# Optimization experiments

Hardware: AMD Instinct MI355X
Metric: run time of the kernel (lower is better)

The kernel has to match this reference:

```python
import jax, jax.numpy as jnp
import numpy as np

N, E = 100000, 1200000
IN, HC = 3, 64
FC1, FC2, FC3, OUT = 64, 32, 16, 3
BN_EPS = 1e-5


def _lin(key, fan_in, fan_out):
    # kaiming-uniform-ish init, zero bias (as in parameter_init)
    bound = np.sqrt(6.0 / fan_in)
    w = jax.random.uniform(key, (fan_in, fan_out), minval=-bound, maxval=bound, dtype=jnp.float32)
    return w, jnp.zeros((fan_out,), jnp.float32)


def setup_inputs() -> dict:
    key = jax.random.key(0)
    ks = jax.random.split(key, 16)
    x = jax.random.normal(ks[0], (N, IN), dtype=jnp.float32)
    edge_index = jax.random.randint(ks[1], (2, E), 0, N, dtype=jnp.int64)
    d = {"x": x, "edge_index": edge_index}
    # EdgeConv MLPs: Linear(2*c_in, hc) -> ReLU -> Linear(hc, hc)
    d["w1a"], d["b1a"] = _lin(ks[2], 2 * IN, HC)
    d["w1b"], d["b1b"] = _lin(ks[3], HC, HC)
    d["w2a"], d["b2a"] = _lin(ks[4], 2 * HC, HC)
    d["w2b"], d["b2b"] = _lin(ks[5], HC, HC)
    d["w3a"], d["b3a"] = _lin(ks[6], 2 * HC, HC)
    d["w3b"], d["b3b"] = _lin(ks[7], HC, HC)
    # BatchNorm (eval mode) params per layer: gamma, beta, running_mean, running_var
    for i in (1, 2, 3):
        d[f"bn{i}_g"] = jnp.ones((HC,), jnp.float32)
        d[f"bn{i}_b"] = jnp.zeros((HC,), jnp.float32)
        d[f"bn{i}_m"] = jnp.zeros((HC,), jnp.float32)
        d[f"bn{i}_v"] = jnp.ones((HC,), jnp.float32)
    # dense head
    d["lw1"], d["lb1"] = _lin(ks[8], HC, FC1)
    d["lw2"], d["lb2"] = _lin(ks[9], FC1, FC2)
    d["lw3"], d["lb3"] = _lin(ks[10], FC2, FC3)
    d["lw4"], d["lb4"] = _lin(ks[11], FC3, OUT)
    return d


def _edge_conv(x, src, dst, wa, ba, wb, bb):
    # PyG EdgeConv: message = mlp(cat[x_i, x_j - x_i]), max-aggregated at target i
    x_i = x[dst]                              # [E, C]
    x_j = x[src]                              # [E, C]
    h = jnp.concatenate([x_i, x_j - x_i], axis=-1)   # [E, 2C]
    h = jax.nn.relu(h @ wa + ba) @ wb + bb           # [E, HC]
    agg = jax.ops.segment_max(h, dst, num_segments=x.shape[0])
    return jnp.where(jnp.isfinite(agg), agg, 0.0)    # isolated nodes -> 0


def _bn(x, g, b, m, v):
    return (x - m) * jax.lax.rsqrt(v + BN_EPS) * g + b


def reference(x, edge_index,
              w1a, b1a, w1b, b1b, w2a, b2a, w2b, b2b, w3a, b3a, w3b, b3b,
              bn1_g, bn1_b, bn1_m, bn1_v, bn2_g, bn2_b, bn2_m, bn2_v,
              bn3_g, bn3_b, bn3_m, bn3_v,
              lw1, lb1, lw2, lb2, lw3, lb3, lw4, lb4):
    src, dst = edge_index[0], edge_index[1]
    h = _edge_conv(x, src, dst, w1a, b1a, w1b, b1b)
    h = jax.nn.relu(_bn(h, bn1_g, bn1_b, bn1_m, bn1_v))
    h = _edge_conv(h, src, dst, w2a, b2a, w2b, b2b)
    h = jax.nn.relu(_bn(h, bn2_g, bn2_b, bn2_m, bn2_v))
    h = _edge_conv(h, src, dst, w3a, b3a, w3b, b3b)
    h = jax.nn.relu(_bn(h, bn3_g, bn3_b, bn3_m, bn3_v))
    h = jax.nn.relu(h @ lw1 + lb1)
    h = jax.nn.relu(h @ lw2 + lb2)
    h = jax.nn.relu(h @ lw3 + lb3)
    return h @ lw4 + lb4
```

## Files before the change

kernel.cpp:

```cpp
#include <hip/hip_runtime.h>

#define CAP 64
#define BN_EPS 1e-5f

typedef _Float16 f16;
typedef _Float16 half8 __attribute__((ext_vector_type(8)));
typedef float f32x4 __attribute__((ext_vector_type(4)));

__global__ __launch_bounds__(256) void build_buckets(
    const int* __restrict__ ei, int E,
    int* __restrict__ deg, int* __restrict__ bucket)
{
    int e = blockIdx.x * blockDim.x + threadIdx.x;
    if (e >= E) return;
    int src = ei[e];
    int dst = ei[E + e];
    int slot = atomicAdd(&deg[dst], 1);
    if (slot < CAP) bucket[dst * CAP + slot] = src;
}

__global__ __launch_bounds__(256) void uv_kernel(
    const float* __restrict__ feat, int ldf, int K, int N,
    const float* __restrict__ wa, const float* __restrict__ ba,
    f16* __restrict__ U, f16* __restrict__ V)
{
    __shared__ float Wlds[2][64][64];
    __shared__ float blds[64];
    int tid = threadIdx.x;
    for (int idx = tid; idx < 2 * K * 64; idx += blockDim.x) {
        int half = idx / (K * 64);
        int rem = idx - half * (K * 64);
        int k = rem >> 6, o = rem & 63;
        float wB = wa[(K + k) * 64 + o];
        Wlds[half][k][o] = (half == 0) ? (wa[k * 64 + o] - wB) : wB;
    }
    if (tid < 64) blds[tid] = ba[tid];
    __syncthreads();

    int t = blockIdx.x * blockDim.x + tid;
    if (t >= 2 * N) return;
    int node = t >> 1, half = t & 1;

    float acc[64];
    #pragma unroll
    for (int o = 0; o < 64; ++o) acc[o] = (half == 0) ? blds[o] : 0.f;

    const float* f = feat + (long)node * ldf;
    for (int k = 0; k < K; ++k) {
        float c = f[k];
        #pragma unroll
        for (int o = 0; o < 64; ++o) acc[o] = fmaf(c, Wlds[half][k][o], acc[o]);
    }
    f16* dstp = (half == 0 ? U : V) + (long)node * 64;
    #pragma unroll
    for (int o = 0; o < 64; o += 8) {
        half8 h;
        #pragma unroll
        for (int j = 0; j < 8; ++j) h[j] = (f16)acc[o + j];
        *(half8*)(dstp + o) = h;
    }
}

__global__ __launch_bounds__(256) void node_kernel(
    const f16* __restrict__ U, const f16* __restrict__ V,
    const int* __restrict__ deg, const int* __restrict__ bucket,
    const float* __restrict__ wb, const float* __restrict__ bb,
    const float* __restrict__ bng, const float* __restrict__ bnb,
    const float* __restrict__ bnm, const float* __restrict__ bnv,
    int N, float* __restrict__ Fout)
{
    const int lane = threadIdx.x & 63;
    const int r16 = lane >> 4, c16 = lane & 15;
    const int wid = (blockIdx.x * blockDim.x + threadIdx.x) >> 6;
    const int nwaves = (gridDim.x * blockDim.x) >> 6;

    half8 bfrag[8];
    #pragma unroll
    for (int ct = 0; ct < 4; ++ct)
        #pragma unroll
        for (int s = 0; s < 2; ++s) {
            half8 h;
            #pragma unroll
            for (int j = 0; j < 8; ++j) {
                int k = 32 * s + 8 * r16 + j;
                h[j] = (f16)wb[k * 64 + 16 * ct + c16];
            }
            bfrag[ct * 2 + s] = h;
        }

    const float bbv = bb[lane];
    const float g = bng[lane], be = bnb[lane];
    const float rs = rsqrtf(bnv[lane] + BN_EPS), mm = bnm[lane];

    int chunk = (N + nwaves - 1) / nwaves;
    int n0 = wid * chunk;
    int n1 = n0 + chunk; if (n1 > N) n1 = N;

    for (int node = n0; node < n1; ++node) {
        int d = deg[node]; if (d > CAP) d = CAP;

        const half8* urow = (const half8*)(U + (long)node * 64);
        half8 u0 = urow[r16];
        half8 u1 = urow[4 + r16];

        float m0 = -INFINITY, m1 = -INFINITY, m2 = -INFINITY, m3 = -INFINITY;
        int ntile = (d + 15) >> 4;
        for (int t = 0; t < ntile; ++t) {
            int slot = t * 16 + c16;
            int src = (slot < d) ? bucket[node * CAP + slot] : 0;
            const half8* vrow = (const half8*)(V + (long)src * 64);
            half8 a0 = vrow[r16] + u0;
            half8 a1 = vrow[4 + r16] + u1;
            #pragma unroll
            for (int j = 0; j < 8; ++j) {
                a0[j] = a0[j] > (f16)0 ? a0[j] : (f16)0;
                a1[j] = a1[j] > (f16)0 ? a1[j] : (f16)0;
            }
            const f32x4 z = {0.f, 0.f, 0.f, 0.f};
            #pragma unroll
            for (int ct = 0; ct < 4; ++ct) {
                f32x4 acc = __builtin_amdgcn_mfma_f32_16x16x32_f16(a0, bfrag[ct * 2 + 0], z, 0, 0, 0);
                acc = __builtin_amdgcn_mfma_f32_16x16x32_f16(a1, bfrag[ct * 2 + 1], acc, 0, 0, 0);
                float mx = -INFINITY;
                #pragma unroll
                for (int r = 0; r < 4; ++r) {
                    int row = t * 16 + r16 * 4 + r;
                    float val = (row < d) ? acc[r] : -INFINITY;
                    mx = fmaxf(mx, val);
                }
                mx = fmaxf(mx, __shfl_xor(mx, 16));
                mx = fmaxf(mx, __shfl_xor(mx, 32));
                if (ct == 0) m0 = fmaxf(m0, mx);
                else if (ct == 1) m1 = fmaxf(m1, mx);
                else if (ct == 2) m2 = fmaxf(m2, mx);
                else m3 = fmaxf(m3, mx);
            }
        }
        float sel = (r16 == 0) ? m0 : (r16 == 1) ? m1 : (r16 == 2) ? m2 : m3;
        float aggv = (d > 0) ? sel + bbv : 0.f;
        float bn = (aggv - mm) * rs * g + be;
        Fout[(long)node * 64 + lane] = fmaxf(bn, 0.f);
    }
}

__global__ __launch_bounds__(256) void head_kernel(
    const float* __restrict__ F,
    const float* __restrict__ lw1, const float* __restrict__ lb1,
    const float* __restrict__ lw2, const float* __restrict__ lb2,
    const float* __restrict__ lw3, const float* __restrict__ lb3,
    const float* __restrict__ lw4, const float* __restrict__ lb4,
    int N, float* __restrict__ out)
{
    __shared__ float W1[64][64];
    __shared__ float W2[64][32];
    __shared__ float W3[32][16];
    __shared__ float W4[16][3];
    __shared__ float B1[64], B2[32], B3[16], B4[3];
    int tid = threadIdx.x;
    for (int i = tid; i < 64 * 64; i += blockDim.x) W1[i >> 6][i & 63] = lw1[i];
    for (int i = tid; i < 64 * 32; i += blockDim.x) W2[i >> 5][i & 31] = lw2[i];
    for (int i = tid; i < 32 * 16; i += blockDim.x) W3[i >> 4][i & 15] = lw3[i];
    for (int i = tid; i < 16 * 3;  i += blockDim.x) W4[i / 3][i % 3]  = lw4[i];
    if (tid < 64) B1[tid] = lb1[tid];
    if (tid < 32) B2[tid] = lb2[tid];
    if (tid < 16) B3[tid] = lb3[tid];
    if (tid < 3)  B4[tid] = lb4[tid];
    __syncthreads();

    int n = blockIdx.x * blockDim.x + tid;
    if (n >= N) return;
    const float* f = F + (long)n * 64;

    float h1[64];
    #pragma unroll
    for (int o = 0; o < 64; ++o) h1[o] = B1[o];
    for (int k = 0; k < 64; ++k) {
        float c = f[k];
        #pragma unroll
        for (int o = 0; o < 64; ++o) h1[o] = fmaf(c, W1[k][o], h1[o]);
    }
    float h2[32];
    #pragma unroll
    for (int o = 0; o < 32; ++o) h2[o] = B2[o];
    #pragma unroll
    for (int k = 0; k < 64; ++k) {
        float c = fmaxf(h1[k], 0.f);
        #pragma unroll
        for (int o = 0; o < 32; ++o) h2[o] = fmaf(c, W2[k][o], h2[o]);
    }
    float h3[16];
    #pragma unroll
    for (int o = 0; o < 16; ++o) h3[o] = B3[o];
    #pragma unroll
    for (int k = 0; k < 32; ++k) {
        float c = fmaxf(h2[k], 0.f);
        #pragma unroll
        for (int o = 0; o < 16; ++o) h3[o] = fmaf(c, W3[k][o], h3[o]);
    }
    float o0 = B4[0], o1 = B4[1], o2 = B4[2];
    #pragma unroll
    for (int k = 0; k < 16; ++k) {
        float c = fmaxf(h3[k], 0.f);
        o0 = fmaf(c, W4[k][0], o0);
        o1 = fmaf(c, W4[k][1], o1);
        o2 = fmaf(c, W4[k][2], o2);
    }
    out[(long)n * 3 + 0] = o0;
    out[(long)n * 3 + 1] = o1;
    out[(long)n * 3 + 2] = o2;
}

extern "C" void kernel_launch(void* const* d_in, const int* in_sizes, int n_in,
                              void* d_out, int out_size, void* d_ws, size_t ws_size,
                              hipStream_t stream)
{
    const float* x   = (const float*)d_in[0];
    const int*   ei  = (const int*)d_in[1];
    int N = in_sizes[0] / 3;
    int E = in_sizes[1] / 2;

    const float* w1a = (const float*)d_in[2];  const float* b1a = (const float*)d_in[3];
    const float* w1b = (const float*)d_in[4];  const float* b1b = (const float*)d_in[5];
    const float* w2a = (const float*)d_in[6];  const float* b2a = (const float*)d_in[7];
    const float* w2b = (const float*)d_in[8];  const float* b2b = (const float*)d_in[9];
    const float* w3a = (const float*)d_in[10]; const float* b3a = (const float*)d_in[11];
    const float* w3b = (const float*)d_in[12]; const float* b3b = (const float*)d_in[13];
    const float* bn1g = (const float*)d_in[14]; const float* bn1b = (const float*)d_in[15];
    const float* bn1m = (const float*)d_in[16]; const float* bn1v = (const float*)d_in[17];
    const float* bn2g = (const float*)d_in[18]; const float* bn2b = (const float*)d_in[19];
    const float* bn2m = (const float*)d_in[20]; const float* bn2v = (const float*)d_in[21];
    const float* bn3g = (const float*)d_in[22]; const float* bn3b = (const float*)d_in[23];
    const float* bn3m = (const float*)d_in[24]; const float* bn3v = (const float*)d_in[25];
    const float* lw1 = (const float*)d_in[26]; const float* lb1 = (const float*)d_in[27];
    const float* lw2 = (const float*)d_in[28]; const float* lb2 = (const float*)d_in[29];
    const float* lw3 = (const float*)d_in[30]; const float* lb3 = (const float*)d_in[31];
    const float* lw4 = (const float*)d_in[32]; const float* lb4 = (const float*)d_in[33];
    float* out = (float*)d_out;

    char* ws = (char*)d_ws;
    size_t off = 0;
    auto alloc = [&](size_t bytes) { void* p = ws + off; off += (bytes + 255) & ~(size_t)255; return p; };
    int*   deg    = (int*)  alloc((size_t)N * sizeof(int));
    int*   bucket = (int*)  alloc((size_t)N * CAP * sizeof(int));
    f16*   U      = (f16*)  alloc((size_t)N * 64 * sizeof(f16));
    f16*   V      = (f16*)  alloc((size_t)N * 64 * sizeof(f16));
    float* F      = (float*)alloc((size_t)N * 64 * sizeof(float));
    (void)ws_size; (void)n_in; (void)out_size;

    hipMemsetAsync(deg, 0, (size_t)N * sizeof(int), stream);
    build_buckets<<<(E + 255) / 256, 256, 0, stream>>>(ei, E, deg, bucket);

    int uv_grid   = (2 * N + 255) / 256;
    int node_blocks = 2048;
    int nd_grid   = (N + 255) / 256;

    uv_kernel<<<uv_grid, 256, 0, stream>>>(x, 3, 3, N, w1a, b1a, U, V);
    node_kernel<<<node_blocks, 256, 0, stream>>>(U, V, deg, bucket, w1b, b1b,
                                                 bn1g, bn1b, bn1m, bn1v, N, F);
    uv_kernel<<<uv_grid, 256, 0, stream>>>(F, 64, 64, N, w2a, b2a, U, V);
    node_kernel<<<node_blocks, 256, 0, stream>>>(U, V, deg, bucket, w2b, b2b,
                                                 bn2g, bn2b, bn2m, bn2v, N, F);
    uv_kernel<<<uv_grid, 256, 0, stream>>>(F, 64, 64, N, w3a, b3a, U, V);
    node_kernel<<<node_blocks, 256, 0, stream>>>(U, V, deg, bucket, w3b, b3b,
                                                 bn3g, bn3b, bn3m, bn3v, N, F);
    head_kernel<<<nd_grid, 256, 0, stream>>>(F, lw1, lb1, lw2, lb2, lw3, lb3,
                                             lw4, lb4, N, out);
}
```

Baseline: 592.2 us.

## Software-pipeline neighbor gathers across nodes in EdgeConv aggregation loop

Restructures the per-wave node loop so the first 16 bucket entries, V rows and U row for the next node are loaded while the current node is processed. A bucket index two nodes ahead is also fetched early, and out-of-range indices are clamped with an unsigned compare. Degrees for the wave's nodes are loaded once into lanes and broadcast with a shuffle. This is meant to hide the dependent global-memory latency of bucket, then V, then U loads. In exchange it uses more registers, and the shuffle-based degree lookup assumes each wave handles at most 64 nodes.

```diff
diff --git a/kernel.cpp b/kernel.cpp
--- a/kernel.cpp
+++ b/kernel.cpp
@@ -95,22 +95,71 @@
     int chunk = (N + nwaves - 1) / nwaves;
     int n0 = wid * chunk;
     int n1 = n0 + chunk; if (n1 > N) n1 = N;
+    if (n0 >= n1) return;
+
+    int dval = 0;
+    if (lane < n1 - n0) dval = deg[n0 + lane];
+    dval = dval > CAP ? CAP : dval;
+
+    int bkt_cur = bucket[(long)n0 * CAP + c16];
+    int np = (n0 + 1 < n1) ? n0 + 1 : n0;
+    int bkt_nxt = bucket[(long)np * CAP + c16];
+
+    unsigned s0u = (unsigned)bkt_cur < (unsigned)N ? (unsigned)bkt_cur : 0u;
+    const half8* vr = (const half8*)(V + (long)s0u * 64);
+    half8 vA = vr[r16], vB = vr[4 + r16];
+    const half8* ur = (const half8*)(U + (long)n0 * 64);
+    half8 uA = ur[r16], uB = ur[4 + r16];
 
     for (int node = n0; node < n1; ++node) {
-        int d = deg[node]; if (d > CAP) d = CAP;
-
-        const half8* urow = (const half8*)(U + (long)node * 64);
-        half8 u0 = urow[r16];
-        half8 u1 = urow[4 + r16];
+        unsigned s1u = (unsigned)bkt_nxt < (unsigned)N ? (unsigned)bkt_nxt : 0u;
+        const half8* vr1 = (const half8*)(V + (long)s1u * 64);
+        half8 vA2 = vr1[r16], vB2 = vr1[4 + r16];
+        int nn = (node + 2 < n1) ? node + 2 : n1 - 1;
+        int bkt_fut = bucket[(long)nn * CAP + c16];
+        int np1 = (node + 1 < n1) ? node + 1 : node;
+        const half8* ur1 = (const half8*)(U + (long)np1 * 64);
+        half8 uA2 = ur1[r16], uB2 = ur1[4 + r16];
+
+        int d = __shfl(dval, node - n0);
 
         float m0 = -INFINITY, m1 = -INFINITY, m2 = -INFINITY, m3 = -INFINITY;
         int ntile = (d + 15) >> 4;
-        for (int t = 0; t < ntile; ++t) {
-            int slot = t * 16 + c16;
-            int src = (slot < d) ? bucket[node * CAP + slot] : 0;
-            const half8* vrow = (const half8*)(V + (long)src * 64);
-            half8 a0 = vrow[r16] + u0;
-            half8 a1 = vrow[4 + r16] + u1;
+
+        if (ntile > 0) {
+            half8 a0 = vA + uA;
+            half8 a1 = vB + uB;
+            #pragma unroll
+            for (int j = 0; j < 8; ++j) {
+                a0[j] = a0[j] > (f16)0 ? a0[j] : (f16)0;
+                a1[j] = a1[j] > (f16)0 ? a1[j] : (f16)0;
+            }
+            const f32x4 z = {0.f, 0.f, 0.f, 0.f};
+            #pragma unroll
+            for (int ct = 0; ct < 4; ++ct) {
+                f32x4 acc = __builtin_amdgcn_mfma_f32_16x16x32_f16(a0, bfrag[ct * 2 + 0], z, 0, 0, 0);
+                acc = __builtin_amdgcn_mfma_f32_16x16x32_f16(a1, bfrag[ct * 2 + 1], acc, 0, 0, 0);
+                float mx = -INFINITY;
+                #pragma unroll
+                for (int r = 0; r < 4; ++r) {
+                    int row = r16 * 4 + r;
+                    float val = (row < d) ? acc[r] : -INFINITY;
+                    mx = fmaxf(mx, val);
+                }
+                mx = fmaxf(mx, __shfl_xor(mx, 16));
+                mx = fmaxf(mx, __shfl_xor(mx, 32));
+                if (ct == 0) m0 = fmaxf(m0, mx);
+                else if (ct == 1) m1 = fmaxf(m1, mx);
+                else if (ct == 2) m2 = fmaxf(m2, mx);
+                else m3 = fmaxf(m3, mx);
+            }
+        }
+        for (int t = 1; t < ntile; ++t) {
+            int bkt = bucket[(long)node * CAP + t * 16 + c16];
+            unsigned su = (unsigned)bkt < (unsigned)N ? (unsigned)bkt : 0u;
+            const half8* vrt = (const half8*)(V + (long)su * 64);
+            half8 a0 = vrt[r16] + uA;
+            half8 a1 = vrt[4 + r16] + uB;
             #pragma unroll
             for (int j = 0; j < 8; ++j) {
                 a0[j] = a0[j] > (f16)0 ? a0[j] : (f16)0;
@@ -136,10 +185,13 @@
                 else m3 = fmaxf(m3, mx);
             }
         }
+
         float sel = (r16 == 0) ? m0 : (r16 == 1) ? m1 : (r16 == 2) ? m2 : m3;
         float aggv = (d > 0) ? sel + bbv : 0.f;
         float bn = (aggv - mm) * rs * g + be;
         Fout[(long)node * 64 + lane] = fmaxf(bn, 0.f);
+
+        vA = vA2; vB = vB2; uA = uA2; uB = uB2; bkt_nxt = bkt_fut;
     }
 }
 
```

Result: faster. 551.2 us (-6.9%).
